# Kernel tuning notes

Hardware: AMD Instinct MI355X
Metric: run time of the kernel (lower is better)

The kernel has to match this reference:

```python
import jax, jax.numpy as jnp
import numpy as np

N_E = 1024
E_DIM = 256
N_TOK = 65536
BETA = 0.25


def setup_inputs() -> dict:
    key = jax.random.key(0)
    k1, k2 = jax.random.split(key)
    z = jax.random.normal(k1, (N_TOK, E_DIM), dtype=jnp.float32)
    # nn.Embedding weight, init uniform(-1/n_e, 1/n_e) in the original; use normal-like scale via uniform
    W = jax.random.uniform(k2, (N_E, E_DIM), dtype=jnp.float32, minval=-1.0 / N_E, maxval=1.0 / N_E)
    return {"z": z, "W": W}


def reference(z, W):
    # cosine distance: d = -normalize(z) @ normalize(W).T  -> (N, n_e)
    zn = z / jnp.linalg.norm(z, axis=-1, keepdims=True)
    Wn = W / jnp.linalg.norm(W, axis=-1, keepdims=True)
    d = -jnp.einsum('nd,ed->ne', zn, Wn)
    min_idx = jnp.argmin(d, axis=1)                       # (N,)
    z_q = W[min_idx]                                       # (N, e_dim)
    # commitment / codebook loss with straight-through style detaches
    loss = jnp.mean((jax.lax.stop_gradient(z) - z_q) ** 2) \
         + BETA * jnp.mean((z - jax.lax.stop_gradient(z_q)) ** 2)
    # pos_indices = unique(min_idx) (sorted); neg = np.delete(arange(n_e), pos) (sorted)
    # emb = cat(W[pos], W[neg]); reproduce with a stable argsort on membership mask
    pos_mask = jnp.zeros((N_E,), dtype=bool).at[min_idx].set(True)
    order = jnp.argsort(jnp.logical_not(pos_mask), stable=True)  # pos (sorted) first, then neg (sorted)
    emb = W[order]                                         # (n_e, e_dim)
    label = pos_mask[order].astype(z.dtype)                # (n_e,)
    return emb, label, loss
```

## Files before the change

kernel.cpp:

```cpp
#include <hip/hip_runtime.h>
#include <math.h>


typedef unsigned short u16;
typedef unsigned int   u32;
typedef unsigned long long u64;
typedef __attribute__((ext_vector_type(8))) short short8;
typedef __attribute__((ext_vector_type(4))) float f32x4;

#define N_E   1024
#define E_DIM 256
#define N_TOK 65536
#define BETA  0.25f
#define CAPL  16
#define CAPG  8
#define D_ADM 0.08f
#define D_FIL 0.09f

#define WS_INVNORM 0
#define WS_NORMW   4096
#define WS_MASK    8192
#define WS_LACC    12288
#define WS_WCNT    14336
#define WS_WSW     16384
#define WS_CNT     540672
#define WS_CAND    802816
#define WS_WLIST   1851392

static __device__ __forceinline__ u16 f2bf(float f) {
    u32 u = __float_as_uint(f);
    return (u16)((u + 0x7FFFu + ((u >> 16) & 1u)) >> 16);
}
static __device__ __forceinline__ u32 keyenc(float f) {
    u32 u = __float_as_uint(f);
    return u ^ (u32)(((int)u >> 31) | 0x80000000);
}
static __device__ __forceinline__ float keydec(u32 k) {
    u32 u = (k & 0x80000000u) ? (k ^ 0x80000000u) : ~k;
    return __uint_as_float(u);
}

__global__ void k_prep(const float* __restrict__ W, u16* __restrict__ Wsw,
                       float* __restrict__ inv_norm, float* __restrict__ normW,
                       int* __restrict__ mask, double* __restrict__ lacc,
                       u32* __restrict__ wcnt) {
    const int n = blockIdx.x;
    const int l = threadIdx.x;
    const float4 v = reinterpret_cast<const float4*>(W + (size_t)n * E_DIM)[l];
    float s = v.x * v.x + v.y * v.y + v.z * v.z + v.w * v.w;
#pragma unroll
    for (int sh = 1; sh < 64; sh <<= 1) s += __shfl_xor(s, sh, 64);
    const float nw = sqrtf(s), inv = 1.0f / nw;
    if (l == 0) {
        inv_norm[n] = inv; normW[n] = nw; mask[n] = 0;
        if (n < 256) lacc[n] = 0.0;
        if (n == 0) *wcnt = 0u;
    }
    const int o = l >> 1;
    const int kc = o >> 2, q = o & 3;
    const size_t base =
        (((((size_t)(n >> 7) * 8 + kc) * 8 + ((n >> 4) & 7)) * 64 +
          (q * 16 + (n & 15))) * 8) + (l & 1) * 4;
    u16* dst = Wsw + base;
    dst[0] = f2bf(v.x * inv);
    dst[1] = f2bf(v.y * inv);
    dst[2] = f2bf(v.z * inv);
    dst[3] = f2bf(v.w * inv);
}

__global__ __launch_bounds__(512, 4)
void k_score(const float* __restrict__ z, const u16* __restrict__ Wsw,
             const float* __restrict__ normW, u16* __restrict__ cand_g,
             u32* __restrict__ cnt_g, int* __restrict__ mask,
             u32* __restrict__ wlist, u32* __restrict__ wcnt,
             double* __restrict__ lacc) {
    __shared__ __align__(16) u16 A_sw[32768];
    __shared__ u32 bestk[128];
    __shared__ u32 cnt[128];
    __shared__ u32 slots[128 * CAPL];

    const int t    = threadIdx.x;
    const int lane = t & 63;
    const int w    = t >> 6;
    const size_t tok_base = (size_t)blockIdx.x * 128;

    if (t < 128) { bestk[t] = 0u; cnt[t] = 0u; }

    float ssq = 0.f;
#pragma unroll
    for (int i = 0; i < 8; i++) {
        const int c = t + 512 * i;
        const int m = c >> 5, o = c & 31;
        const float* zp = z + (tok_base + m) * E_DIM + o * 8;
        const float4 v0 = reinterpret_cast<const float4*>(zp)[0];
        const float4 v1 = reinterpret_cast<const float4*>(zp)[1];
        ssq += v0.x * v0.x + v0.y * v0.y + v0.z * v0.z + v0.w * v0.w
             + v1.x * v1.x + v1.y * v1.y + v1.z * v1.z + v1.w * v1.w;
        uint4 d;
        d.x = (u32)f2bf(v0.x) | ((u32)f2bf(v0.y) << 16);
        d.y = (u32)f2bf(v0.z) | ((u32)f2bf(v0.w) << 16);
        d.z = (u32)f2bf(v1.x) | ((u32)f2bf(v1.y) << 16);
        d.w = (u32)f2bf(v1.z) | ((u32)f2bf(v1.w) << 16);
        const int kc = o >> 2, q = o & 3, col = m & 15, mt = m >> 4;
        *reinterpret_cast<uint4*>(A_sw + ((size_t)((kc * 8 + mt) * 64 + q * 16 + col)) * 8) = d;
    }
#pragma unroll
    for (int sh = 1; sh < 64; sh <<= 1) ssq += __shfl_xor(ssq, sh, 64);
    if (lane == 0) atomicAdd(&lacc[(blockIdx.x * 8 + w) & 255], (double)ssq);
    __syncthreads();

    const int mq = w >> 2;
    const int nq = w & 3;
    const int q = lane >> 4, col = lane & 15;
    const u16* wb = Wsw + ((size_t)((nq >> 1) * 64 + (nq & 1) * 4)) * 512
                        + (size_t)lane * 8;

#pragma unroll 1
    for (int nb2 = 0; nb2 < 4; nb2++) {
        f32x4 acc[4][4];
#pragma unroll
        for (int mi = 0; mi < 4; mi++)
#pragma unroll
            for (int ni = 0; ni < 4; ni++) {
                f32x4 zf = {0.f, 0.f, 0.f, 0.f};
                acc[mi][ni] = zf;
            }

#pragma unroll 2
        for (int kc = 0; kc < 8; kc++) {
            short8 bf[4], af[4];
#pragma unroll
            for (int ni = 0; ni < 4; ni++)
                bf[ni] = *reinterpret_cast<const short8*>(
                    wb + (size_t)(nb2 * 128 + kc * 8 + ni) * 512);
#pragma unroll
            for (int mi = 0; mi < 4; mi++)
                af[mi] = *reinterpret_cast<const short8*>(
                    A_sw + ((size_t)((kc * 8 + mq * 4 + mi) * 64 + lane)) * 8);
#pragma unroll
            for (int mi = 0; mi < 4; mi++)
#pragma unroll
                for (int ni = 0; ni < 4; ni++)
                    acc[mi][ni] = __builtin_amdgcn_mfma_f32_16x16x32_bf16(
                        af[mi], bf[ni], acc[mi][ni], 0, 0, 0);
        }

#pragma unroll
        for (int mi = 0; mi < 4; mi++)
#pragma unroll
            for (int r = 0; r < 4; r++) {
                float m0 = fmaxf(fmaxf(acc[mi][0][r], acc[mi][1][r]),
                                 fmaxf(acc[mi][2][r], acc[mi][3][r]));
#pragma unroll
                for (int sh = 1; sh < 16; sh <<= 1)
                    m0 = fmaxf(m0, __shfl_xor(m0, sh, 64));
                if (col == 0)
                    atomicMax(&bestk[mq * 64 + mi * 16 + q * 4 + r], keyenc(m0));
            }
        __syncthreads();

#pragma unroll
        for (int mi = 0; mi < 4; mi++)
#pragma unroll
            for (int r = 0; r < 4; r++) {
                const int tk = mq * 64 + mi * 16 + q * 4 + r;
                const float thr = keydec(bestk[tk]) - D_ADM;
#pragma unroll
                for (int ni = 0; ni < 4; ni++) {
                    const float v = acc[mi][ni][r];
                    if (v >= thr) {
                        const int code = (nb2 * 16 + nq * 4 + ni) * 16 + col;
                        const u32 sl = atomicAdd(&cnt[tk], 1u);
                        if (sl < CAPL) {
                            const float vc = fminf(fmaxf((v + 16.f) * 2048.f, 0.f), 65535.f);
                            slots[tk * CAPL + sl] = ((u32)vc << 16) | (u32)code;
                        }
                    }
                }
            }
    }

    __syncthreads();
    if (t < 128) {
        const size_t tokg = tok_base + t;
        const u32 c = cnt[t];
        const float best = keydec(bestk[t]);
        bool amb = false;
        float xacc = 0.f;
        if (c > CAPL) {
            cnt_g[tokg] = 0xFFFFFFFFu; amb = true;
        } else {
            const float thrf = best - D_FIL;
            u16 loc[CAPG]; u32 m = 0;
            for (u32 i = 0; i < c; i++) {
                const u32 s2 = slots[t * CAPL + i];
                const float ap = (float)(s2 >> 16) * (1.0f / 2048.0f) - 16.0f;
                if (ap >= thrf) { if (m < CAPG) loc[m] = (u16)(s2 & 0xFFFFu); m++; }
            }
            if (m == 1) {
                const int bi = loc[0];
                mask[bi] = 1;
                const float nw = normW[bi];
                xacc = fmaf(-2.0f * best, nw, nw * nw);
            } else if (m <= CAPG) {
                for (u32 i = 0; i < m; i++) cand_g[tokg * CAPG + i] = loc[i];
                cnt_g[tokg] = m; amb = true;
            } else {
                cnt_g[tokg] = 0xFFFFFFFFu; amb = true;
            }
        }
        const u64 bal = __ballot(amb);
        u32 base = 0;
        if (lane == 0) base = atomicAdd(wcnt, (u32)__popcll(bal));
        base = (u32)__shfl((int)base, 0, 64);
        if (amb) wlist[base + (u32)__popcll(bal & ((1ull << lane) - 1ull))] = (u32)tokg;
        float xs = xacc;
#pragma unroll
        for (int sh = 1; sh < 64; sh <<= 1) xs += __shfl_xor(xs, sh, 64);
        if (lane == 0) atomicAdd(&lacc[(blockIdx.x * 2 + w) & 255], (double)xs);
    }
}

__global__ __launch_bounds__(256)
void k_pick(const float* __restrict__ z, const float* __restrict__ W,
            const float* __restrict__ inv_norm, const float* __restrict__ normW,
            const u16* __restrict__ cand_g, const u32* __restrict__ cnt_g,
            const u32* __restrict__ wlist, const u32* __restrict__ wcnt,
            int* __restrict__ mask, double* __restrict__ lacc) {
    const int t = threadIdx.x, lane = t & 63;
    const int gl = t & 15, grp = t >> 4;
    const u32 total = *wcnt;
    float xs = 0.f;
    for (u32 i = blockIdx.x * 16 + grp; i < total; i += 2048 * 16) {
        const size_t tok = wlist[i];
        float4 zv[4];
#pragma unroll
        for (int j = 0; j < 4; j++)
            zv[j] = reinterpret_cast<const float4*>(z + tok * E_DIM)[j * 16 + gl];
        const u32 sc = cnt_g[tok];
        const bool full = (sc == 0xFFFFFFFFu);
        const int n_it = full ? N_E : (int)sc;
        float bv = -3.4e38f, bp = 0.f;
        int bi = 0x7FFFFFFF;
#pragma unroll 1
        for (int k2 = 0; k2 < n_it; k2++) {
            const int c = full ? k2 : (int)cand_g[tok * CAPG + k2];
            float p = 0.f;
#pragma unroll
            for (int j = 0; j < 4; j++) {
                const float4 wv = reinterpret_cast<const float4*>(W + (size_t)c * E_DIM)[j * 16 + gl];
                p += zv[j].x * wv.x + zv[j].y * wv.y + zv[j].z * wv.z + zv[j].w * wv.w;
            }
#pragma unroll
            for (int sh = 1; sh < 16; sh <<= 1) p += __shfl_xor(p, sh, 64);
            const float s = p * inv_norm[c];
            if (s > bv || (s == bv && c < bi)) { bv = s; bi = c; bp = p; }
        }
        if (gl == 0) {
            mask[bi] = 1;
            xs += fmaf(-2.0f, bp, normW[bi] * normW[bi]);
        }
    }
    xs += __shfl_xor(xs, 16, 64);
    xs += __shfl_xor(xs, 32, 64);
    if (lane == 0) atomicAdd(&lacc[(blockIdx.x * 4 + (t >> 6)) & 255], (double)xs);
}

__global__ __launch_bounds__(256)
void k_emit(const float* __restrict__ W, const int* __restrict__ mask,
            const double* __restrict__ lacc, float* __restrict__ out) {
    __shared__ int    redp[256], redt[256];
    __shared__ double dred[256];
    const int e = blockIdx.x;
    const int t = threadIdx.x;
    const int4 mv = reinterpret_cast<const int4*>(mask)[t];
    const int b = t * 4;
    redt[t] = mv.x + mv.y + mv.z + mv.w;
    redp[t] = (b + 0 < e ? mv.x : 0) + (b + 1 < e ? mv.y : 0) +
              (b + 2 < e ? mv.z : 0) + (b + 3 < e ? mv.w : 0);
    if (e == 0) dred[t] = lacc[t];
    __syncthreads();
#pragma unroll
    for (int s2 = 128; s2 > 0; s2 >>= 1) {
        if (t < s2) {
            redp[t] += redp[t + s2];
            redt[t] += redt[t + s2];
            if (e == 0) dred[t] += dred[t + s2];
        }
        __syncthreads();
    }
    const int prefix = redp[0], total = redt[0];
    const int m = mask[e];
    const int r = m ? prefix : (total + e - prefix);
    out[(size_t)r * E_DIM + t] = W[(size_t)e * E_DIM + t];
    if (t == 0) out[(size_t)N_E * E_DIM + r] = m ? 1.0f : 0.0f;
    if (e == 0 && t == 0) {
        const double mse = dred[0] / (double)((size_t)N_TOK * E_DIM);
        out[(size_t)N_E * E_DIM + N_E] = (float)((1.0 + (double)BETA) * mse);
    }
}

extern "C" void kernel_launch(void* const* d_in, const int* in_sizes, int n_in,
                              void* d_out, int out_size, void* d_ws, size_t ws_size,
                              hipStream_t stream) {
    const float* z = (const float*)d_in[0];
    const float* W = (const float*)d_in[1];
    float* out = (float*)d_out;
    char* ws = (char*)d_ws;

    float*  inv_norm = (float*)(ws + WS_INVNORM);
    float*  normW    = (float*)(ws + WS_NORMW);
    int*    mask     = (int*)(ws + WS_MASK);
    double* lacc     = (double*)(ws + WS_LACC);
    u32*    wcnt     = (u32*)(ws + WS_WCNT);
    u16*    Wsw      = (u16*)(ws + WS_WSW);
    u32*    cnt      = (u32*)(ws + WS_CNT);
    u16*    cand     = (u16*)(ws + WS_CAND);
    u32*    wlist    = (u32*)(ws + WS_WLIST);

    k_prep <<<N_E, 64, 0, stream>>>(W, Wsw, inv_norm, normW, mask, lacc, wcnt);
    k_score<<<N_TOK / 128, 512, 0, stream>>>(z, Wsw, normW, cand, cnt, mask,
                                             wlist, wcnt, lacc);
    k_pick <<<2048, 256, 0, stream>>>(z, W, inv_norm, normW, cand, cnt,
                                      wlist, wcnt, mask, lacc);
    k_emit <<<N_E, 256, 0, stream>>>(W, mask, lacc, out);
}
```

Measured before the change: 159.2 us.

## Drop per-chunk max reduction and barriers after first code chunk; use packed bf16 convert

The per-chunk shuffle max-reduction and __syncthreads are kept only for the first 256-code chunk. Later chunks admit candidates against the running best threshold and raise bestk via atomicMax on admitted values only. This removes three barriers and the shuffle reductions. Because later thresholds can be stale, more candidates may be admitted, so CAPL is raised to 20, which grows LDS slot storage. The z-to-bf16 conversion also switches to a packed intrinsic, and the k-loop unroll goes from 2 to 4.

```diff
diff --git a/kernel.cpp b/kernel.cpp
--- a/kernel.cpp
+++ b/kernel.cpp
@@ -1,4 +1,5 @@
 #include <hip/hip_runtime.h>
+#include <hip/hip_bf16.h>
 #include <math.h>
 
 
@@ -12,7 +13,7 @@
 #define E_DIM 256
 #define N_TOK 65536
 #define BETA  0.25f
-#define CAPL  16
+#define CAPL  20
 #define CAPG  8
 #define D_ADM 0.08f
 #define D_FIL 0.09f
@@ -30,6 +31,10 @@
 static __device__ __forceinline__ u16 f2bf(float f) {
     u32 u = __float_as_uint(f);
     return (u16)((u + 0x7FFFu + ((u >> 16) & 1u)) >> 16);
+}
+static __device__ __forceinline__ u32 pk2bf(float a, float b) {
+    __hip_bfloat162 p = __float22bfloat162_rn(make_float2(a, b));
+    return *reinterpret_cast<u32*>(&p);
 }
 static __device__ __forceinline__ u32 keyenc(float f) {
     u32 u = __float_as_uint(f);
@@ -97,10 +102,10 @@
         ssq += v0.x * v0.x + v0.y * v0.y + v0.z * v0.z + v0.w * v0.w
              + v1.x * v1.x + v1.y * v1.y + v1.z * v1.z + v1.w * v1.w;
         uint4 d;
-        d.x = (u32)f2bf(v0.x) | ((u32)f2bf(v0.y) << 16);
-        d.y = (u32)f2bf(v0.z) | ((u32)f2bf(v0.w) << 16);
-        d.z = (u32)f2bf(v1.x) | ((u32)f2bf(v1.y) << 16);
-        d.w = (u32)f2bf(v1.z) | ((u32)f2bf(v1.w) << 16);
+        d.x = pk2bf(v0.x, v0.y);
+        d.y = pk2bf(v0.z, v0.w);
+        d.z = pk2bf(v1.x, v1.y);
+        d.w = pk2bf(v1.z, v1.w);
         const int kc = o >> 2, q = o & 3, col = m & 15, mt = m >> 4;
         *reinterpret_cast<uint4*>(A_sw + ((size_t)((kc * 8 + mt) * 64 + q * 16 + col)) * 8) = d;
     }
@@ -115,70 +120,69 @@
     const u16* wb = Wsw + ((size_t)((nq >> 1) * 64 + (nq & 1) * 4)) * 512
                         + (size_t)lane * 8;
 
+    f32x4 acc[4][4];
+
+#define ZERO_ACC() { _Pragma("unroll") for (int mi = 0; mi < 4; mi++) \
+    _Pragma("unroll") for (int ni = 0; ni < 4; ni++) { \
+        f32x4 zf = {0.f, 0.f, 0.f, 0.f}; acc[mi][ni] = zf; } }
+
+#define KLOOP(NB2) { \
+    _Pragma("unroll 4") \
+    for (int kc = 0; kc < 8; kc++) { \
+        short8 bf[4], af[4]; \
+        _Pragma("unroll") for (int ni = 0; ni < 4; ni++) \
+            bf[ni] = *reinterpret_cast<const short8*>( \
+                wb + (size_t)((NB2) * 128 + kc * 8 + ni) * 512); \
+        _Pragma("unroll") for (int mi = 0; mi < 4; mi++) \
+            af[mi] = *reinterpret_cast<const short8*>( \
+                A_sw + ((size_t)((kc * 8 + mq * 4 + mi) * 64 + lane)) * 8); \
+        _Pragma("unroll") for (int mi = 0; mi < 4; mi++) \
+        _Pragma("unroll") for (int ni = 0; ni < 4; ni++) \
+            acc[mi][ni] = __builtin_amdgcn_mfma_f32_16x16x32_bf16( \
+                af[mi], bf[ni], acc[mi][ni], 0, 0, 0); } }
+
+#define ADMIT(NB2, DO_MAX) { \
+    _Pragma("unroll") for (int mi = 0; mi < 4; mi++) \
+    _Pragma("unroll") for (int r = 0; r < 4; r++) { \
+        const int tk = mq * 64 + mi * 16 + q * 4 + r; \
+        const float thr = keydec(bestk[tk]) - D_ADM; \
+        _Pragma("unroll") for (int ni = 0; ni < 4; ni++) { \
+            const float v = acc[mi][ni][r]; \
+            if (v >= thr) { \
+                if (DO_MAX) atomicMax(&bestk[tk], keyenc(v)); \
+                const int code = ((NB2) * 16 + nq * 4 + ni) * 16 + col; \
+                const u32 sl = atomicAdd(&cnt[tk], 1u); \
+                if (sl < CAPL) { \
+                    const float vc = fminf(fmaxf((v + 16.f) * 2048.f, 0.f), 65535.f); \
+                    slots[tk * CAPL + sl] = ((u32)vc << 16) | (u32)code; \
+                } } } } }
+
+    ZERO_ACC();
+    KLOOP(0);
+#pragma unroll
+    for (int mi = 0; mi < 4; mi++)
+#pragma unroll
+        for (int r = 0; r < 4; r++) {
+            float m0 = fmaxf(fmaxf(acc[mi][0][r], acc[mi][1][r]),
+                             fmaxf(acc[mi][2][r], acc[mi][3][r]));
+#pragma unroll
+            for (int sh = 1; sh < 16; sh <<= 1)
+                m0 = fmaxf(m0, __shfl_xor(m0, sh, 64));
+            if (col == 0)
+                atomicMax(&bestk[mq * 64 + mi * 16 + q * 4 + r], keyenc(m0));
+        }
+    __syncthreads();
+    ADMIT(0, 0);
+
 #pragma unroll 1
-    for (int nb2 = 0; nb2 < 4; nb2++) {
-        f32x4 acc[4][4];
-#pragma unroll
-        for (int mi = 0; mi < 4; mi++)
-#pragma unroll
-            for (int ni = 0; ni < 4; ni++) {
-                f32x4 zf = {0.f, 0.f, 0.f, 0.f};
-                acc[mi][ni] = zf;
-            }
-
-#pragma unroll 2
-        for (int kc = 0; kc < 8; kc++) {
-            short8 bf[4], af[4];
-#pragma unroll
-            for (int ni = 0; ni < 4; ni++)
-                bf[ni] = *reinterpret_cast<const short8*>(
-                    wb + (size_t)(nb2 * 128 + kc * 8 + ni) * 512);
-#pragma unroll
-            for (int mi = 0; mi < 4; mi++)
-                af[mi] = *reinterpret_cast<const short8*>(
-                    A_sw + ((size_t)((kc * 8 + mq * 4 + mi) * 64 + lane)) * 8);
-#pragma unroll
-            for (int mi = 0; mi < 4; mi++)
-#pragma unroll
-                for (int ni = 0; ni < 4; ni++)
-                    acc[mi][ni] = __builtin_amdgcn_mfma_f32_16x16x32_bf16(
-                        af[mi], bf[ni], acc[mi][ni], 0, 0, 0);
-        }
-
-#pragma unroll
-        for (int mi = 0; mi < 4; mi++)
-#pragma unroll
-            for (int r = 0; r < 4; r++) {
-                float m0 = fmaxf(fmaxf(acc[mi][0][r], acc[mi][1][r]),
-                                 fmaxf(acc[mi][2][r], acc[mi][3][r]));
-#pragma unroll
-                for (int sh = 1; sh < 16; sh <<= 1)
-                    m0 = fmaxf(m0, __shfl_xor(m0, sh, 64));
-                if (col == 0)
-                    atomicMax(&bestk[mq * 64 + mi * 16 + q * 4 + r], keyenc(m0));
-            }
-        __syncthreads();
-
-#pragma unroll
-        for (int mi = 0; mi < 4; mi++)
-#pragma unroll
-            for (int r = 0; r < 4; r++) {
-                const int tk = mq * 64 + mi * 16 + q * 4 + r;
-                const float thr = keydec(bestk[tk]) - D_ADM;
-#pragma unroll
-                for (int ni = 0; ni < 4; ni++) {
-                    const float v = acc[mi][ni][r];
-                    if (v >= thr) {
-                        const int code = (nb2 * 16 + nq * 4 + ni) * 16 + col;
-                        const u32 sl = atomicAdd(&cnt[tk], 1u);
-                        if (sl < CAPL) {
-                            const float vc = fminf(fmaxf((v + 16.f) * 2048.f, 0.f), 65535.f);
-                            slots[tk * CAPL + sl] = ((u32)vc << 16) | (u32)code;
-                        }
-                    }
-                }
-            }
-    }
+    for (int nb2 = 1; nb2 < 4; nb2++) {
+        ZERO_ACC();
+        KLOOP(nb2);
+        ADMIT(nb2, 1);
+    }
+#undef ZERO_ACC
+#undef KLOOP
+#undef ADMIT
 
     __syncthreads();
     if (t < 128) {
```

Measured after the change: 209.6 us. +31.7%, slower.
